# Performance work log

Measured on AMD Instinct MI355X. Metric: run time of the kernel, lower is better.

## Reference

```python
import jax, jax.numpy as jnp
import numpy as np

NEIGHBOUR = 3  # matches init_kwargs['neighbour']


def _conv2d(x, w, b=None, stride=1, pad=0):
    out = jax.lax.conv_general_dilated(
        x, w, (stride, stride), [(pad, pad), (pad, pad)],
        dimension_numbers=('NCHW', 'OIHW', 'NCHW'))
    if b is not None:
        out = out + b[None, :, None, None]
    return out


def _warp(x, offset, wg_w, wg_b, conv_w):
    """Deformable bilinear warp: offsets -> 4 corner gathers -> modulate -> regroup -> strided conv."""
    k = NEIGHBOUR
    N = k * k
    B, C, H, W = x.shape
    m = jax.nn.sigmoid(_conv2d(x, wg_w, wg_b, 1, 1))          # [B,N,H,W] modulation gate
    xp = jnp.pad(x, ((0, 0), (0, 0), (1, 1), (1, 1)))         # zero pad -> [B,C,H+2,W+2]
    Hp, Wp = H + 2, W + 2
    r = jnp.arange(-(k - 1) // 2, (k - 1) // 2 + 1, dtype=x.dtype)
    pnx, pny = jnp.meshgrid(r, r, indexing='ij')              # kernel-neighbour offsets p_n
    # absolute sampling positions in padded coords (p_0 starts at 1 due to padding)
    p0x = jnp.arange(1, H + 1, dtype=x.dtype)[None, :, None, None]
    p0y = jnp.arange(1, W + 1, dtype=x.dtype)[None, None, :, None]
    off = offset.transpose(0, 2, 3, 1)                        # [B,H,W,2N]; first N = x, last N = y
    px = p0x + pnx.ravel()[None, None, None, :] + off[..., :N]  # [B,H,W,N]
    py = p0y + pny.ravel()[None, None, None, :] + off[..., N:]
    fx = jnp.floor(jax.lax.stop_gradient(px))                 # p.detach().floor()
    fy = jnp.floor(jax.lax.stop_gradient(py))
    qx_lt = jnp.clip(fx, 0, Hp - 1)
    qy_lt = jnp.clip(fy, 0, Wp - 1)
    qx_rb = jnp.clip(fx + 1, 0, Hp - 1)
    qy_rb = jnp.clip(fy + 1, 0, Wp - 1)
    px = jnp.clip(px, 0, Hp - 1)
    py = jnp.clip(py, 0, Wp - 1)
    # bilinear weights (same algebra as the torch code)
    g_lt = (1 + (qx_lt - px)) * (1 + (qy_lt - py))
    g_rb = (1 - (qx_rb - px)) * (1 - (qy_rb - py))
    g_lb = (1 + (qx_lt - px)) * (1 - (qy_rb - py))
    g_rt = (1 - (qx_rb - px)) * (1 + (qy_lt - py))
    ix_lt = qx_lt.astype(jnp.int32); iy_lt = qy_lt.astype(jnp.int32)
    ix_rb = qx_rb.astype(jnp.int32); iy_rb = qy_rb.astype(jnp.int32)
    x_flat = xp.reshape(B, C, Hp * Wp)

    def gather(ix, iy):
        idx = (ix * Wp + iy).reshape(B, 1, H * W * N)
        return jnp.take_along_axis(x_flat, idx, axis=-1).reshape(B, C, H, W, N)

    xw = (g_lt[:, None] * gather(ix_lt, iy_lt)
          + g_rb[:, None] * gather(ix_rb, iy_rb)
          + g_lb[:, None] * gather(ix_lt, iy_rb)
          + g_rt[:, None] * gather(ix_rb, iy_lt))              # [B,C,H,W,N]
    xw = xw * m.transpose(0, 2, 3, 1)[:, None]                 # modulation, broadcast over C
    # regroup [B,C,H,W,k,k] -> [B,C,H*k,W*k] (matches _reshape_x_warped ordering)
    xw = xw.reshape(B, C, H, W, k, k).transpose(0, 1, 2, 4, 3, 5).reshape(B, C, H * k, W * k)
    return _conv2d(xw, conv_w, None, stride=k, pad=0)          # grouped-back strided conv


def setup_inputs() -> dict:
    B, C, MH, H, W = 4, 64, 18, 128, 128  # MH = 2*neighbour^2
    key = jax.random.key(0)
    ks = jax.random.split(key, 12)
    f32 = jnp.float32
    s = 0.05  # weight scale to keep gates unsaturated
    return {
        'x_t': jax.random.normal(ks[0], (B, C, H, W), f32),
        'pre_offset': jax.random.normal(ks[1], (B, MH, H, W), f32),
        'mean': jax.random.normal(ks[2], (B, MH, H, W), f32),
        'upd_w': s * jax.random.normal(ks[3], (MH, C + MH, 3, 3), f32),
        'upd_b': s * jax.random.normal(ks[4], (MH,), f32),
        'rst_w': s * jax.random.normal(ks[5], (MH, C + MH, 3, 3), f32),
        'rst_b': s * jax.random.normal(ks[6], (MH,), f32),
        'out_w': s * jax.random.normal(ks[7], (MH, C + MH, 3, 3), f32),
        'out_b': s * jax.random.normal(ks[8], (MH,), f32),
        'wg_w': s * jax.random.normal(ks[9], (9, C, 3, 3), f32),
        'wg_b': s * jax.random.normal(ks[10], (9,), f32),
        'warp_conv_w': s * jax.random.normal(ks[11], (C, C, 3, 3), f32),
    }


def reference(x_t, pre_offset, mean, upd_w, upd_b, rst_w, rst_b, out_w, out_b,
              wg_w, wg_b, warp_conv_w):
    stacked = jnp.concatenate([x_t, pre_offset], axis=1)
    update_gate = jax.nn.sigmoid(_conv2d(stacked, upd_w, upd_b, 1, 1))
    reset_gate = jax.nn.sigmoid(_conv2d(stacked, rst_w, rst_b, 1, 1))
    cand = jnp.tanh(_conv2d(jnp.concatenate([x_t, pre_offset * reset_gate], axis=1), out_w, out_b, 1, 1))
    offset = pre_offset * (1 - update_gate) + cand * update_gate
    mean_new = mean + 0.5 * (pre_offset - mean)
    offset = offset + mean_new
    x_out = _warp(x_t, offset, wg_w, wg_b, warp_conv_w)
    return (x_out, offset, mean_new)
```

## Files before the change

### kernel.cpp

```cpp
#include <hip/hip_runtime.h>
#include <hip/hip_bf16.h>
#include <math.h>

#define Bn  4
#define Cc  64
#define MHc 18
#define Hh  128
#define Wd  128
#define HW  (Hh*Wd)
#define Np  9
#define HP  130
#define WP  130
#define XPE (HP*WP*Cc)
#define PPE (HP*WP*32)
#define KX  576
#define KP  288
#define KT  (KX+KP)

typedef __attribute__((ext_vector_type(8))) short short8;
typedef __attribute__((ext_vector_type(4))) float float4v;

__device__ __forceinline__ float bf2f(__hip_bfloat16 x) { return __bfloat162float(x); }
__device__ __forceinline__ __hip_bfloat16 f2bf(float x) { return __float2bfloat16(x); }
__device__ __forceinline__ float sigm(float x) { return 1.f / (1.f + expf(-x)); }
__device__ __forceinline__ float s2f(short s) {
  return __uint_as_float(((unsigned)(unsigned short)s) << 16);
}
__device__ __forceinline__ short f2bs(float x) {
  __hip_bfloat16 h = __float2bfloat16(x);
  return *reinterpret_cast<short*>(&h);
}

#define NW1 (64*KT)
#define NW2 (32*KP)
#define NW3 (Cc*Cc*Np)

__global__ __launch_bounds__(256)
void k_prep(const float* __restrict__ x, const float* __restrict__ po,
            const float* __restrict__ upd_w, const float* __restrict__ rst_w,
            const float* __restrict__ out_w, const float* __restrict__ wg_w,
            const float* __restrict__ wcw,
            __hip_bfloat16* __restrict__ xp, __hip_bfloat16* __restrict__ pp,
            __hip_bfloat16* __restrict__ wall, __hip_bfloat16* __restrict__ w2,
            __hip_bfloat16* __restrict__ wt) {
  __shared__ float tile[16][65];
  int blk = blockIdx.x;
  int t = threadIdx.x;
  if (blk < 4096) {
    int wtile = blk & 7;
    int h = (blk >> 3) & 127;
    int b = blk >> 10;
    int w0 = wtile * 16;
    int wa = t & 15, cq = t >> 4;
    #pragma unroll
    for (int j = 0; j < 4; ++j) {
      int c = cq * 4 + j;
      tile[wa][c] = x[(b*Cc + c)*HW + h*Wd + w0 + wa];
    }
    __syncthreads();
    int cb = t & 63, wq = t >> 6;
    #pragma unroll
    for (int j = 0; j < 4; ++j) {
      int w = wq * 4 + j;
      xp[b*XPE + ((h+1)*WP + (w0 + w + 1))*Cc + cb] = f2bf(tile[w][cb]);
    }
  } else if (blk < 4608) {
    int pb = blk - 4096;
    int h = pb & 127;
    int b = pb >> 7;
    int w = t & 127;
    int half = t >> 7;
    for (int j = 0; j < 9; ++j) {
      int ch = half * 9 + j;
      float v = po[(b*MHc + ch)*HW + h*Wd + w];
      pp[b*PPE + ((h+1)*WP + (w+1))*32 + ch] = f2bf(v);
    }
  } else {
    int idx = (blk - 4608) * 256 + t;
    if (idx < NW1) {
      int k  = idx % KT;
      int gr = idx / KT;
      float v = 0.f;
      if (k < KX) {
        int n = k >> 6, ci = k & 63;
        if      (gr < 18) v = upd_w[(gr*(Cc+MHc) + ci)*9 + n];
        else if (gr < 36) v = rst_w[((gr-18)*(Cc+MHc) + ci)*9 + n];
        else if (gr < 54) v = out_w[((gr-36)*(Cc+MHc) + ci)*9 + n];
        else if (gr < 63) v = wg_w[((gr-54)*Cc + ci)*9 + n];
      } else {
        int kk = k - KX;
        int n = kk >> 5, jc = kk & 31;
        if (jc < 18) {
          if      (gr < 18) v = upd_w[(gr*(Cc+MHc) + Cc + jc)*9 + n];
          else if (gr < 36) v = rst_w[((gr-18)*(Cc+MHc) + Cc + jc)*9 + n];
        }
      }
      wall[idx] = f2bf(v);
    } else if (idx < NW1 + NW2) {
      int i2 = idx - NW1;
      int k  = i2 % KP;
      int oc = i2 / KP;
      int n = k >> 5, jc = k & 31;
      float v = (oc < 18 && jc < 18) ? out_w[(oc*(Cc+MHc) + Cc + jc)*9 + n] : 0.f;
      w2[i2] = f2bf(v);
    } else if (idx < NW1 + NW2 + NW3) {
      int i3 = idx - NW1 - NW2;
      int k  = i3 % 576;
      int co = i3 / 576;
      wt[i3] = f2bf(wcw[(co*Cc + (k & 63))*9 + (k >> 6)]);
    }
  }
}

__global__ __launch_bounds__(256)
void k_gates(const __hip_bfloat16* __restrict__ xpad,
             const __hip_bfloat16* __restrict__ popad,
             const __hip_bfloat16* __restrict__ wall,
             const float* __restrict__ po,
             const float* __restrict__ upd_b,
             const float* __restrict__ rst_b,
             const float* __restrict__ out_b,
             const float* __restrict__ wg_b,
             float* __restrict__ u_out,
             float* __restrict__ cx_out,
             __hip_bfloat16* __restrict__ ropad,
             __hip_bfloat16* __restrict__ m_t) {
  __shared__ __align__(16) char winx[6912];
  __shared__ __align__(16) char winp[3456];
  __shared__ __align__(16) __hip_bfloat16 roL[16][32];
  int blk = blockIdx.x;
  int wtile = blk & 7;
  int h = (blk >> 3) & 127;
  int b = blk >> 10;
  int w0 = wtile * 16;
  int lane = threadIdx.x & 63;
  int wave = threadIdx.x >> 6;
  int t = threadIdx.x;

  ((unsigned int*)roL)[t] = 0u;

  const __hip_bfloat16* xpb = xpad + b * XPE;
  const __hip_bfloat16* ppb = popad + b * PPE;

  for (int i = t; i < 432; i += 256) {
    int r = i / 144, cidx = i - r * 144;
    short8 v = *reinterpret_cast<const short8*>(
        xpb + ((h + r) * WP + w0) * Cc + cidx * 8);
    int o = i * 16;
    *reinterpret_cast<short8*>(winx + (o ^ (((o >> 7) & 7) << 4))) = v;
  }
  if (t < 216) {
    int r = t / 72, cidx = t - r * 72;
    short8 v = *reinterpret_cast<const short8*>(
        ppb + ((h + r) * WP + w0) * 32 + cidx * 8);
    int o = t * 16;
    *reinterpret_cast<short8*>(winp + (o ^ (((o >> 6) & 3) << 4))) = v;
  }
  __syncthreads();

  int mrow = lane & 15;
  int quad = lane >> 4;
  int cotile = wave * 16;
  float4v acc = {0.f, 0.f, 0.f, 0.f};
  #pragma unroll
  for (int ks = 0; ks < KT/32; ++ks) {
    short8 a = *reinterpret_cast<const short8*>(
        wall + (cotile + mrow) * KT + ks * 32 + quad * 8);
    short8 bfr;
    if (ks < 18) {
      int n = ks >> 1;
      int rowidx = (n / 3) * 18 + mrow + (n % 3);
      int lin = rowidx * 128 + (ks & 1) * 64 + quad * 16;
      bfr = *reinterpret_cast<const short8*>(winx + (lin ^ ((rowidx & 7) << 4)));
    } else {
      int n = ks - 18;
      int rowidx = (n / 3) * 18 + mrow + (n % 3);
      int lin = rowidx * 64 + quad * 16;
      bfr = *reinterpret_cast<const short8*>(winp + (lin ^ ((rowidx & 3) << 4)));
    }
    acc = __builtin_amdgcn_mfma_f32_16x16x32_bf16(a, bfr, acc, 0, 0, 0);
  }

  int sp = h * Wd + w0 + mrow;
  #pragma unroll
  for (int r = 0; r < 4; ++r) {
    int gr = cotile + quad * 4 + r;
    float v = acc[r];
    if (gr < 18) {
      u_out[(b*MHc + gr)*HW + sp] = sigm(v + upd_b[gr]);
    } else if (gr < 36) {
      int oc = gr - 18;
      float rr = sigm(v + rst_b[oc]);
      roL[mrow][oc] = f2bf(rr * po[(b*MHc + oc)*HW + sp]);
    } else if (gr < 54) {
      int oc = gr - 36;
      cx_out[(b*MHc + oc)*HW + sp] = v + out_b[oc];
    } else if (gr < 63) {
      int nn = gr - 54;
      m_t[(b*HW + sp)*9 + nn] = f2bf(sigm(v + wg_b[nn]));
    }
  }
  __syncthreads();
  unsigned int* dst = (unsigned int*)(ropad + b*PPE + ((h+1)*WP + (w0+1))*32);
  dst[t] = ((unsigned int*)roL)[t];
}

__global__ __launch_bounds__(256)
void k_fuse(const __hip_bfloat16* __restrict__ xpad,
            const __hip_bfloat16* __restrict__ ropad,
            const __hip_bfloat16* __restrict__ w2,
            const __hip_bfloat16* __restrict__ wt,
            const __hip_bfloat16* __restrict__ m_t,
            const float* __restrict__ po,
            const float* __restrict__ mean,
            float* __restrict__ out_off,
            float* __restrict__ out_mn,
            float* __restrict__ out_x) {
  __shared__ __align__(16) char lbuf[16*584*2];
  __shared__ float offL[16][18];
  __shared__ float mL[16][9];
  __shared__ __align__(16) float gw[144][4];
  __shared__ __align__(16) int   gb[144][2];
  auto xw = (__hip_bfloat16(*)[584])lbuf;

  int blk = blockIdx.x;
  int wtile = blk & 7;
  int h = (blk >> 3) & 127;
  int b = blk >> 10;
  int w0 = wtile * 16;
  int lane = threadIdx.x & 63;
  int wave = threadIdx.x >> 6;
  int t = threadIdx.x;

  const __hip_bfloat16* rpb = ropad + b * PPE;
  if (t < 216) {
    int r = t / 72, cidx = t - r * 72;
    short8 v = *reinterpret_cast<const short8*>(
        rpb + ((h + r) * WP + w0) * 32 + cidx * 8);
    int o = t * 16;
    *reinterpret_cast<short8*>(lbuf + (o ^ (((o >> 6) & 3) << 4))) = v;
  }
  __syncthreads();

  int mrow = lane & 15;
  int quad = lane >> 4;

  if (wave < 2) {
    float4v acc = {0.f, 0.f, 0.f, 0.f};
    #pragma unroll
    for (int ks = 0; ks < KP/32; ++ks) {
      short8 a = *reinterpret_cast<const short8*>(
          w2 + (wave*16 + mrow) * KP + ks * 32 + quad * 8);
      int rowidx = (ks / 3) * 18 + mrow + (ks % 3);
      int lin = rowidx * 64 + quad * 16;
      short8 bfr = *reinterpret_cast<const short8*>(
          lbuf + (lin ^ ((rowidx & 3) << 4)));
      acc = __builtin_amdgcn_mfma_f32_16x16x32_bf16(a, bfr, acc, 0, 0, 0);
    }
    int sp = h * Wd + w0 + mrow;
    #pragma unroll
    for (int r = 0; r < 4; ++r) {
      int gr = wave*16 + quad * 4 + r;
      if (gr < 18) {
        int gi = (b*MHc + gr)*HW + sp;
        float cand = tanhf(out_off[gi] + acc[r]);
        float u = out_mn[gi];
        float p = po[gi];
        float mn = 0.5f * (mean[gi] + p);
        float off = p * (1.f - u) + cand * u + mn;
        out_off[gi] = off;
        out_mn[gi]  = mn;
        offL[mrow][gr] = off;
      }
    }
  } else {
    int base = (wave - 2) * 64 + lane;
    #pragma unroll
    for (int rep = 0; rep < 2; ++rep) {
      int id = base + rep * 128;
      if (id < 144) {
        int px = id / 9, n = id % 9;
        mL[px][n] = bf2f(m_t[(b*HW + h*Wd + w0 + px)*9 + n]);
      }
    }
  }
  __syncthreads();

  if (t < 144) {
    int px = t / 9;
    int n = t - px * 9;
    int wp = w0 + px;
    float ox = offL[px][n];
    float oy = offL[px][9 + n];
    float mnv = mL[px][n];
    float px_ = (float)(h + 1) + (float)(n / 3 - 1) + ox;
    float py_ = (float)(wp + 1) + (float)(n % 3 - 1) + oy;
    float fx = floorf(px_), fy = floorf(py_);
    float xlt = fminf(fmaxf(fx,       0.f), 129.f);
    float ylt = fminf(fmaxf(fy,       0.f), 129.f);
    float xrb = fminf(fmaxf(fx + 1.f, 0.f), 129.f);
    float yrb = fminf(fmaxf(fy + 1.f, 0.f), 129.f);
    float pxc = fminf(fmaxf(px_, 0.f), 129.f);
    float pyc = fminf(fmaxf(py_, 0.f), 129.f);
    float glt = (1.f + xlt - pxc) * (1.f + ylt - pyc);
    float grb = (1.f - xrb + pxc) * (1.f - yrb + pyc);
    float glb = (1.f + xlt - pxc) * (1.f - yrb + pyc);
    float grt = (1.f - xrb + pxc) * (1.f + ylt - pyc);
    int ixl = (int)xlt, iyl = (int)ylt, ixr = (int)xrb, iyr = (int)yrb;
    bool yAdj = (iyr == iyl + 1);
    gw[t][0] = (glt + (yAdj ? 0.f : glb)) * mnv;
    gw[t][1] = (yAdj ? glb : 0.f) * mnv;
    gw[t][2] = (grt + (yAdj ? 0.f : grb)) * mnv;
    gw[t][3] = (yAdj ? grb : 0.f) * mnv;
    gb[t][0] = (ixl * WP + iyl) * Cc;
    gb[t][1] = (ixr * WP + iyl) * Cc;
  }
  __syncthreads();

  const __hip_bfloat16* xpb = xpad + b * XPE;
  for (int it = t; it < 1152; it += 256) {
    int q  = it >> 3;
    int c0 = (it & 7) * 8;
    float4v g = *reinterpret_cast<const float4v*>(gw[q]);
    int bL = gb[q][0], bR = gb[q][1];
    short8 l0 = *reinterpret_cast<const short8*>(xpb + bL + c0);
    short8 l1 = *reinterpret_cast<const short8*>(xpb + bL + 64 + c0);
    short8 r0 = *reinterpret_cast<const short8*>(xpb + bR + c0);
    short8 r1 = *reinterpret_cast<const short8*>(xpb + bR + 64 + c0);
    short8 ov;
    #pragma unroll
    for (int j = 0; j < 8; ++j) {
      float vv = g.x * s2f(l0[j]);
      vv = fmaf(g.y, s2f(l1[j]), vv);
      vv = fmaf(g.z, s2f(r0[j]), vv);
      vv = fmaf(g.w, s2f(r1[j]), vv);
      ov[j] = f2bs(vv);
    }
    int pl = q / 9;
    int n  = q - pl * 9;
    *reinterpret_cast<short8*>(&xw[pl][n * 64 + c0]) = ov;
  }
  __syncthreads();

  int cotile = wave * 16;
  float4v acc = {0.f, 0.f, 0.f, 0.f};
  for (int ks = 0; ks < 18; ++ks) {
    short8 a = *reinterpret_cast<const short8*>(
        wt + (cotile + mrow) * 576 + ks * 32 + quad * 8);
    short8 bfr = *reinterpret_cast<const short8*>(
        &xw[mrow][ks * 32 + quad * 8]);
    acc = __builtin_amdgcn_mfma_f32_16x16x32_bf16(a, bfr, acc, 0, 0, 0);
  }
  #pragma unroll
  for (int r = 0; r < 4; ++r) {
    int co = cotile + quad * 4 + r;
    out_x[((b * Cc + co) * Hh + h) * Wd + w0 + mrow] = acc[r];
  }
}

__global__ void f_convAB(const float* __restrict__ x, const float* __restrict__ po,
                         const float* __restrict__ wA, const float* __restrict__ bA,
                         const float* __restrict__ wB, const float* __restrict__ bB,
                         float* __restrict__ u_scr, float* __restrict__ ro_scr) {
  int idx = blockIdx.x * 256 + threadIdx.x;
  if (idx >= Bn * MHc * HW) return;
  int w = idx & 127, h = (idx >> 7) & 127, oc = (idx >> 14) % MHc, b = idx / (MHc*HW);
  float accA = bA[oc], accB = bB[oc];
  const float* xb = x + b*Cc*HW; const float* pb = po + b*MHc*HW;
  for (int ic = 0; ic < Cc + MHc; ++ic) {
    const float* src = (ic < Cc) ? (xb + ic*HW) : (pb + (ic-Cc)*HW);
    const float* wa = wA + (oc*(Cc+MHc)+ic)*9; const float* wb = wB + (oc*(Cc+MHc)+ic)*9;
    for (int kh = 0; kh < 3; ++kh) { int hh = h+kh-1; if ((unsigned)hh >= Hh) continue;
      for (int kw = 0; kw < 3; ++kw) { int ww = w+kw-1; if ((unsigned)ww >= Wd) continue;
        float v = src[hh*Wd+ww]; accA += v*wa[kh*3+kw]; accB += v*wb[kh*3+kw]; } }
  }
  u_scr[idx] = sigm(accA); ro_scr[idx] = sigm(accB) * pb[oc*HW + h*Wd + w];
}
__global__ void f_convC(const float* __restrict__ x, const float* __restrict__ po,
                        const float* __restrict__ mean, const float* __restrict__ wC,
                        const float* __restrict__ bC, const float* __restrict__ u_scr,
                        const float* __restrict__ ro_scr, float* __restrict__ out_off,
                        float* __restrict__ out_mean) {
  int idx = blockIdx.x * 256 + threadIdx.x;
  if (idx >= Bn * MHc * HW) return;
  int w = idx & 127, h = (idx >> 7) & 127, oc = (idx >> 14) % MHc, b = idx / (MHc*HW);
  float acc = bC[oc];
  const float* xb = x + b*Cc*HW; const float* rb = ro_scr + b*MHc*HW;
  for (int ic = 0; ic < Cc + MHc; ++ic) {
    const float* src = (ic < Cc) ? (xb + ic*HW) : (rb + (ic-Cc)*HW);
    const float* wv = wC + (oc*(Cc+MHc)+ic)*9;
    for (int kh = 0; kh < 3; ++kh) { int hh = h+kh-1; if ((unsigned)hh >= Hh) continue;
      for (int kw = 0; kw < 3; ++kw) { int ww = w+kw-1; if ((unsigned)ww >= Wd) continue;
        acc += src[hh*Wd+ww]*wv[kh*3+kw]; } }
  }
  float cand = tanhf(acc); float u = u_scr[idx]; float p = po[idx];
  float mn = 0.5f*(mean[idx]+p);
  out_off[idx] = p*(1.f-u)+cand*u+mn; out_mean[idx] = mn;
}
__global__ __launch_bounds__(256)
void f_warp(const float* __restrict__ x, const float* __restrict__ off_f,
            const float* __restrict__ wg, const float* __restrict__ bg,
            const float* __restrict__ wc, float* __restrict__ out) {
  __shared__ float mred[4][Np][64]; __shared__ float mval[4][Np];
  __shared__ float xwv[4][Np][64];
  int lane = threadIdx.x & 63, wave = threadIdx.x >> 6;
  int p = blockIdx.x * 4 + wave;
  int b = p >> 14, rem = p & 16383, h = rem >> 7, w = rem & 127;
  const float* xc = x + (b*Cc + lane)*HW;
  float part[Np];
  for (int n = 0; n < Np; ++n) part[n] = 0.f;
  for (int kh = 0; kh < 3; ++kh) { int hh = h+kh-1; if ((unsigned)hh >= Hh) continue;
    for (int kw = 0; kw < 3; ++kw) { int ww = w+kw-1; if ((unsigned)ww >= Wd) continue;
      float v = xc[hh*Wd+ww];
      for (int n = 0; n < Np; ++n) part[n] += v*wg[(n*Cc+lane)*9+kh*3+kw]; } }
  for (int n = 0; n < Np; ++n) mred[wave][n][lane] = part[n];
  __syncthreads();
  if (lane < Np) { float s = bg[lane];
    for (int c = 0; c < Cc; ++c) s += mred[wave][lane][c];
    mval[wave][lane] = sigm(s); }
  __syncthreads();
  const float* offb = off_f + b*MHc*HW; int sp = h*Wd + w;
  for (int n = 0; n < Np; ++n) {
    float px = (float)(h+1) + (float)(n/3-1) + offb[n*HW+sp];
    float py = (float)(w+1) + (float)(n%3-1) + offb[(9+n)*HW+sp];
    float fxq = floorf(px), fyq = floorf(py);
    float xlt = fminf(fmaxf(fxq,0.f),129.f), ylt = fminf(fmaxf(fyq,0.f),129.f);
    float xrb = fminf(fmaxf(fxq+1.f,0.f),129.f), yrb = fminf(fmaxf(fyq+1.f,0.f),129.f);
    float pxc = fminf(fmaxf(px,0.f),129.f), pyc = fminf(fmaxf(py,0.f),129.f);
    float glt = (1.f+xlt-pxc)*(1.f+ylt-pyc), grb = (1.f-xrb+pxc)*(1.f-yrb+pyc);
    float glb = (1.f+xlt-pxc)*(1.f-yrb+pyc), grt = (1.f-xrb+pxc)*(1.f+ylt-pyc);
    int ixl=(int)xlt, iyl=(int)ylt, ixr=(int)xrb, iyr=(int)yrb;
    float vlt=0.f,vrb=0.f,vlb=0.f,vrt=0.f;
    if (ixl>=1&&ixl<=Hh&&iyl>=1&&iyl<=Wd) vlt = xc[(ixl-1)*Wd+(iyl-1)];
    if (ixr>=1&&ixr<=Hh&&iyr>=1&&iyr<=Wd) vrb = xc[(ixr-1)*Wd+(iyr-1)];
    if (ixl>=1&&ixl<=Hh&&iyr>=1&&iyr<=Wd) vlb = xc[(ixl-1)*Wd+(iyr-1)];
    if (ixr>=1&&ixr<=Hh&&iyl>=1&&iyl<=Wd) vrt = xc[(ixr-1)*Wd+(iyl-1)];
    xwv[wave][n][lane] = (glt*vlt+grb*vrb+glb*vlb+grt*vrt)*mval[wave][n];
  }
  __syncthreads();
  float acc = 0.f;
  for (int c = 0; c < Cc; ++c)
    for (int n = 0; n < Np; ++n)
      acc += xwv[wave][n][c]*wc[(lane*Cc+c)*9+n];
  out[(b*Cc+lane)*HW + h*Wd + w] = acc;
}

extern "C" void kernel_launch(void* const* d_in, const int* in_sizes, int n_in,
                              void* d_out, int out_size, void* d_ws, size_t ws_size,
                              hipStream_t stream) {
  (void)in_sizes; (void)n_in; (void)out_size;
  const float* x_t   = (const float*)d_in[0];
  const float* po    = (const float*)d_in[1];
  const float* mean  = (const float*)d_in[2];
  const float* upd_w = (const float*)d_in[3];
  const float* upd_b = (const float*)d_in[4];
  const float* rst_w = (const float*)d_in[5];
  const float* rst_b = (const float*)d_in[6];
  const float* out_w = (const float*)d_in[7];
  const float* out_b = (const float*)d_in[8];
  const float* wg_w  = (const float*)d_in[9];
  const float* wg_b  = (const float*)d_in[10];
  const float* wcw   = (const float*)d_in[11];

  float* out_x   = (float*)d_out;
  float* out_off = out_x + 4194304;
  float* out_mn  = out_off + 1179648;

  char* ws = (char*)d_ws;
  __hip_bfloat16* xpad  = (__hip_bfloat16*)(ws + 0);
  __hip_bfloat16* popad = (__hip_bfloat16*)(ws + 8652800);
  __hip_bfloat16* ropad = (__hip_bfloat16*)(ws + 12979200);
  __hip_bfloat16* wall  = (__hip_bfloat16*)(ws + 17305600);
  __hip_bfloat16* w2    = (__hip_bfloat16*)(ws + 17416192);
  __hip_bfloat16* wt_bf = (__hip_bfloat16*)(ws + 17434624);
  __hip_bfloat16* m_t   = (__hip_bfloat16*)(ws + 17508352);
  const size_t WS_NEED = 18688000;

  if (ws_size >= WS_NEED) {
    hipMemsetAsync(d_ws, 0, 17305600, stream);
    hipLaunchKernelGGL(k_prep,  dim3(5004), dim3(256), 0, stream,
                       x_t, po, upd_w, rst_w, out_w, wg_w, wcw,
                       xpad, popad, wall, w2, wt_bf);
    hipLaunchKernelGGL(k_gates, dim3(4096), dim3(256), 0, stream,
                       xpad, popad, wall, po, upd_b, rst_b, out_b, wg_b,
                       out_mn, out_off, ropad, m_t);
    hipLaunchKernelGGL(k_fuse,  dim3(4096), dim3(256), 0, stream,
                       xpad, ropad, w2, wt_bf, m_t, po, mean,
                       out_off, out_mn, out_x);
  } else {
    float* u_scr  = out_x;
    float* cx_scr = out_x + 1179648;
    hipLaunchKernelGGL(f_convAB, dim3(4608), dim3(256), 0, stream,
                       x_t, po, upd_w, upd_b, rst_w, rst_b, u_scr, cx_scr);
    hipLaunchKernelGGL(f_convC,  dim3(4608), dim3(256), 0, stream,
                       x_t, po, mean, out_w, out_b, u_scr, cx_scr,
                       out_off, out_mn);
    hipLaunchKernelGGL(f_warp,   dim3(16384), dim3(256), 0, stream,
                       x_t, out_off, wg_w, wg_b, wcw, out_x);
  }
}
```

Measured before the change: 203.1 us.

## Restructure k_fuse so each wave owns 16 pixels without block barriers

k_fuse now runs 128-thread blocks, and each wave handles its own 16-pixel strip end to end. A wave computes the candidate conv with MFMA straight from global ropad, then the bilinear coefficients in per-wave shared slots. It builds the warped B-fragments in registers and feeds them directly into four MFMA accumulators covering all 64 output channels. This removes the staged LDS tiles and all __syncthreads, trading them for redundant global weight loads per wave and higher register pressure.

```diff
diff --git a/kernel.cpp b/kernel.cpp
--- a/kernel.cpp
+++ b/kernel.cpp
@@ -205,7 +205,7 @@
   dst[t] = ((unsigned int*)roL)[t];
 }
 
-__global__ __launch_bounds__(256)
+__global__ __launch_bounds__(128)
 void k_fuse(const __hip_bfloat16* __restrict__ xpad,
             const __hip_bfloat16* __restrict__ ropad,
             const __hip_bfloat16* __restrict__ w2,
@@ -216,145 +216,137 @@
             float* __restrict__ out_off,
             float* __restrict__ out_mn,
             float* __restrict__ out_x) {
-  __shared__ __align__(16) char lbuf[16*584*2];
-  __shared__ float offL[16][18];
-  __shared__ float mL[16][9];
-  __shared__ __align__(16) float gw[144][4];
-  __shared__ __align__(16) int   gb[144][2];
-  auto xw = (__hip_bfloat16(*)[584])lbuf;
+  __shared__ float offW[2][16][18];
+  __shared__ __align__(16) float gwW[2][144][4];
+  __shared__ __align__(8)  int   gbW[2][144][2];
 
   int blk = blockIdx.x;
-  int wtile = blk & 7;
-  int h = (blk >> 3) & 127;
-  int b = blk >> 10;
-  int w0 = wtile * 16;
+  int wtile = blk & 3;
+  int h = (blk >> 2) & 127;
+  int b = blk >> 9;
   int lane = threadIdx.x & 63;
-  int wave = threadIdx.x >> 6;
-  int t = threadIdx.x;
-
-  const __hip_bfloat16* rpb = ropad + b * PPE;
-  if (t < 216) {
-    int r = t / 72, cidx = t - r * 72;
-    short8 v = *reinterpret_cast<const short8*>(
-        rpb + ((h + r) * WP + w0) * 32 + cidx * 8);
-    int o = t * 16;
-    *reinterpret_cast<short8*>(lbuf + (o ^ (((o >> 6) & 3) << 4))) = v;
-  }
-  __syncthreads();
+  int wv = threadIdx.x >> 6;
+  int wq0 = wtile * 32 + wv * 16;
 
   int mrow = lane & 15;
   int quad = lane >> 4;
 
-  if (wave < 2) {
-    float4v acc = {0.f, 0.f, 0.f, 0.f};
-    #pragma unroll
-    for (int ks = 0; ks < KP/32; ++ks) {
-      short8 a = *reinterpret_cast<const short8*>(
-          w2 + (wave*16 + mrow) * KP + ks * 32 + quad * 8);
-      int rowidx = (ks / 3) * 18 + mrow + (ks % 3);
-      int lin = rowidx * 64 + quad * 16;
-      short8 bfr = *reinterpret_cast<const short8*>(
-          lbuf + (lin ^ ((rowidx & 3) << 4)));
-      acc = __builtin_amdgcn_mfma_f32_16x16x32_bf16(a, bfr, acc, 0, 0, 0);
-    }
-    int sp = h * Wd + w0 + mrow;
+  const __hip_bfloat16* rpb = ropad + b * PPE;
+  float4v acc2a = {0.f,0.f,0.f,0.f}, acc2b = {0.f,0.f,0.f,0.f};
+  #pragma unroll
+  for (int ks = 0; ks < 9; ++ks) {
+    short8 bfr = *reinterpret_cast<const short8*>(
+        rpb + ((h + ks/3) * WP + wq0 + mrow + ks%3) * 32 + quad * 8);
+    short8 a0 = *reinterpret_cast<const short8*>(
+        w2 + mrow * KP + ks * 32 + quad * 8);
+    short8 a1 = *reinterpret_cast<const short8*>(
+        w2 + (16 + mrow) * KP + ks * 32 + quad * 8);
+    acc2a = __builtin_amdgcn_mfma_f32_16x16x32_bf16(a0, bfr, acc2a, 0, 0, 0);
+    acc2b = __builtin_amdgcn_mfma_f32_16x16x32_bf16(a1, bfr, acc2b, 0, 0, 0);
+  }
+
+  int sp = h * Wd + wq0 + mrow;
+  #pragma unroll
+  for (int am = 0; am < 2; ++am) {
+    float4v av = am ? acc2b : acc2a;
     #pragma unroll
     for (int r = 0; r < 4; ++r) {
-      int gr = wave*16 + quad * 4 + r;
+      int gr = am*16 + quad * 4 + r;
       if (gr < 18) {
         int gi = (b*MHc + gr)*HW + sp;
-        float cand = tanhf(out_off[gi] + acc[r]);
+        float cand = tanhf(out_off[gi] + av[r]);
         float u = out_mn[gi];
         float p = po[gi];
         float mn = 0.5f * (mean[gi] + p);
         float off = p * (1.f - u) + cand * u + mn;
         out_off[gi] = off;
         out_mn[gi]  = mn;
-        offL[mrow][gr] = off;
+        offW[wv][mrow][gr] = off;
       }
     }
-  } else {
-    int base = (wave - 2) * 64 + lane;
-    #pragma unroll
-    for (int rep = 0; rep < 2; ++rep) {
-      int id = base + rep * 128;
-      if (id < 144) {
-        int px = id / 9, n = id % 9;
-        mL[px][n] = bf2f(m_t[(b*HW + h*Wd + w0 + px)*9 + n]);
-      }
-    }
-  }
-  __syncthreads();
-
-  if (t < 144) {
-    int px = t / 9;
-    int n = t - px * 9;
-    int wp = w0 + px;
-    float ox = offL[px][n];
-    float oy = offL[px][9 + n];
-    float mnv = mL[px][n];
-    float px_ = (float)(h + 1) + (float)(n / 3 - 1) + ox;
-    float py_ = (float)(wp + 1) + (float)(n % 3 - 1) + oy;
-    float fx = floorf(px_), fy = floorf(py_);
-    float xlt = fminf(fmaxf(fx,       0.f), 129.f);
-    float ylt = fminf(fmaxf(fy,       0.f), 129.f);
-    float xrb = fminf(fmaxf(fx + 1.f, 0.f), 129.f);
-    float yrb = fminf(fmaxf(fy + 1.f, 0.f), 129.f);
-    float pxc = fminf(fmaxf(px_, 0.f), 129.f);
-    float pyc = fminf(fmaxf(py_, 0.f), 129.f);
-    float glt = (1.f + xlt - pxc) * (1.f + ylt - pyc);
-    float grb = (1.f - xrb + pxc) * (1.f - yrb + pyc);
-    float glb = (1.f + xlt - pxc) * (1.f - yrb + pyc);
-    float grt = (1.f - xrb + pxc) * (1.f + ylt - pyc);
-    int ixl = (int)xlt, iyl = (int)ylt, ixr = (int)xrb, iyr = (int)yrb;
-    bool yAdj = (iyr == iyl + 1);
-    gw[t][0] = (glt + (yAdj ? 0.f : glb)) * mnv;
-    gw[t][1] = (yAdj ? glb : 0.f) * mnv;
-    gw[t][2] = (grt + (yAdj ? 0.f : grb)) * mnv;
-    gw[t][3] = (yAdj ? grb : 0.f) * mnv;
-    gb[t][0] = (ixl * WP + iyl) * Cc;
-    gb[t][1] = (ixr * WP + iyl) * Cc;
-  }
-  __syncthreads();
+  }
+
+  const __hip_bfloat16* mtb = m_t + (size_t)(b*HW + h*Wd + wq0) * 9;
+  #pragma unroll
+  for (int rep = 0; rep < 3; ++rep) {
+    int id = lane + rep * 64;
+    if (id < 144) {
+      int px = id / 9;
+      int n = id - px * 9;
+      int wp = wq0 + px;
+      float ox = offW[wv][px][n];
+      float oy = offW[wv][px][9 + n];
+      float mnv = bf2f(mtb[px * 9 + n]);
+      float px_ = (float)(h + 1) + (float)(n / 3 - 1) + ox;
+      float py_ = (float)(wp + 1) + (float)(n % 3 - 1) + oy;
+      float fx = floorf(px_), fy = floorf(py_);
+      float xlt = fminf(fmaxf(fx,       0.f), 129.f);
+      float ylt = fminf(fmaxf(fy,       0.f), 129.f);
+      float xrb = fminf(fmaxf(fx + 1.f, 0.f), 129.f);
+      float yrb = fminf(fmaxf(fy + 1.f, 0.f), 129.f);
+      float pxc = fminf(fmaxf(px_, 0.f), 129.f);
+      float pyc = fminf(fmaxf(py_, 0.f), 129.f);
+      float glt = (1.f + xlt - pxc) * (1.f + ylt - pyc);
+      float grb = (1.f - xrb + pxc) * (1.f - yrb + pyc);
+      float glb = (1.f + xlt - pxc) * (1.f - yrb + pyc);
+      float grt = (1.f - xrb + pxc) * (1.f + ylt - pyc);
+      int ixl = (int)xlt, iyl = (int)ylt, ixr = (int)xrb, iyr = (int)yrb;
+      bool yAdj = (iyr == iyl + 1);
+      gwW[wv][id][0] = (glt + (yAdj ? 0.f : glb)) * mnv;
+      gwW[wv][id][1] = (yAdj ? glb : 0.f) * mnv;
+      gwW[wv][id][2] = (grt + (yAdj ? 0.f : grb)) * mnv;
+      gwW[wv][id][3] = (yAdj ? grb : 0.f) * mnv;
+      gbW[wv][id][0] = (ixl * WP + iyl) * Cc;
+      gbW[wv][id][1] = (ixr * WP + iyl) * Cc;
+    }
+  }
 
   const __hip_bfloat16* xpb = xpad + b * XPE;
-  for (int it = t; it < 1152; it += 256) {
-    int q  = it >> 3;
-    int c0 = (it & 7) * 8;
-    float4v g = *reinterpret_cast<const float4v*>(gw[q]);
-    int bL = gb[q][0], bR = gb[q][1];
-    short8 l0 = *reinterpret_cast<const short8*>(xpb + bL + c0);
-    short8 l1 = *reinterpret_cast<const short8*>(xpb + bL + 64 + c0);
-    short8 r0 = *reinterpret_cast<const short8*>(xpb + bR + c0);
-    short8 r1 = *reinterpret_cast<const short8*>(xpb + bR + 64 + c0);
-    short8 ov;
+  float4v acc0 = {0.f,0.f,0.f,0.f}, acc1 = {0.f,0.f,0.f,0.f};
+  float4v acc2 = {0.f,0.f,0.f,0.f}, acc3 = {0.f,0.f,0.f,0.f};
+  int q0 = mrow * 9;
+  int cbase = quad * 8;
+  #pragma unroll
+  for (int ks = 0; ks < 18; ++ks) {
+    int q = q0 + (ks >> 1);
+    float4v g = *reinterpret_cast<const float4v*>(gwW[wv][q]);
+    int co = ((ks & 1) << 5) + cbase;
+    int bL = gbW[wv][q][0] + co;
+    int bR = gbW[wv][q][1] + co;
+    short8 l0 = *reinterpret_cast<const short8*>(xpb + bL);
+    short8 l1 = *reinterpret_cast<const short8*>(xpb + bL + 64);
+    short8 r0 = *reinterpret_cast<const short8*>(xpb + bR);
+    short8 r1 = *reinterpret_cast<const short8*>(xpb + bR + 64);
+    short8 bfr;
     #pragma unroll
     for (int j = 0; j < 8; ++j) {
       float vv = g.x * s2f(l0[j]);
       vv = fmaf(g.y, s2f(l1[j]), vv);
       vv = fmaf(g.z, s2f(r0[j]), vv);
       vv = fmaf(g.w, s2f(r1[j]), vv);
-      ov[j] = f2bs(vv);
-    }
-    int pl = q / 9;
-    int n  = q - pl * 9;
-    *reinterpret_cast<short8*>(&xw[pl][n * 64 + c0]) = ov;
-  }
-  __syncthreads();
-
-  int cotile = wave * 16;
-  float4v acc = {0.f, 0.f, 0.f, 0.f};
-  for (int ks = 0; ks < 18; ++ks) {
-    short8 a = *reinterpret_cast<const short8*>(
-        wt + (cotile + mrow) * 576 + ks * 32 + quad * 8);
-    short8 bfr = *reinterpret_cast<const short8*>(
-        &xw[mrow][ks * 32 + quad * 8]);
-    acc = __builtin_amdgcn_mfma_f32_16x16x32_bf16(a, bfr, acc, 0, 0, 0);
+      bfr[j] = f2bs(vv);
+    }
+    short8 a0 = *reinterpret_cast<const short8*>(
+        wt + (0*16 + mrow) * 576 + ks * 32 + cbase);
+    short8 a1 = *reinterpret_cast<const short8*>(
+        wt + (1*16 + mrow) * 576 + ks * 32 + cbase);
+    short8 a2 = *reinterpret_cast<const short8*>(
+        wt + (2*16 + mrow) * 576 + ks * 32 + cbase);
+    short8 a3 = *reinterpret_cast<const short8*>(
+        wt + (3*16 + mrow) * 576 + ks * 32 + cbase);
+    acc0 = __builtin_amdgcn_mfma_f32_16x16x32_bf16(a0, bfr, acc0, 0, 0, 0);
+    acc1 = __builtin_amdgcn_mfma_f32_16x16x32_bf16(a1, bfr, acc1, 0, 0, 0);
+    acc2 = __builtin_amdgcn_mfma_f32_16x16x32_bf16(a2, bfr, acc2, 0, 0, 0);
+    acc3 = __builtin_amdgcn_mfma_f32_16x16x32_bf16(a3, bfr, acc3, 0, 0, 0);
   }
   #pragma unroll
   for (int r = 0; r < 4; ++r) {
-    int co = cotile + quad * 4 + r;
-    out_x[((b * Cc + co) * Hh + h) * Wd + w0 + mrow] = acc[r];
+    float4v* accp[4] = {&acc0, &acc1, &acc2, &acc3};
+    #pragma unroll
+    for (int ct = 0; ct < 4; ++ct) {
+      int co = ct * 16 + quad * 4 + r;
+      out_x[((b * Cc + co) * Hh + h) * Wd + wq0 + mrow] = (*accp[ct])[r];
+    }
   }
 }
 
@@ -484,7 +476,7 @@
     hipLaunchKernelGGL(k_gates, dim3(4096), dim3(256), 0, stream,
                        xpad, popad, wall, po, upd_b, rst_b, out_b, wg_b,
                        out_mn, out_off, ropad, m_t);
-    hipLaunchKernelGGL(k_fuse,  dim3(4096), dim3(256), 0, stream,
+    hipLaunchKernelGGL(k_fuse,  dim3(2048), dim3(128), 0, stream,
                        xpad, ropad, w2, wt_bf, m_t, po, mean,
                        out_off, out_mn, out_x);
   } else {
```

Result: slower. 215.2 us (+6.0%).

## Batch global loads ahead of use and transpose modulation layout across kernels

Applied to the files above, without the earlier changes.

Vectorizes the input transpose in the prep kernel (float4 reads, packed bf16 pair writes) and hoists global loads into registers before computation in the conv, fuse, and gather stages. The gather loop issues all corner loads for five iterations up front, then blends, which puts more loads in flight. The modulation buffer moves to a channel-major layout, so its load in the fuse kernel is coalesced and runs before the first barrier. The cost is higher register pressure, which may lower occupancy.

```diff
diff --git a/kernel.cpp b/kernel.cpp
--- a/kernel.cpp
+++ b/kernel.cpp
@@ -29,6 +29,9 @@
 __device__ __forceinline__ short f2bs(float x) {
   __hip_bfloat16 h = __float2bfloat16(x);
   return *reinterpret_cast<short*>(&h);
+}
+__device__ __forceinline__ unsigned pack2(float lo, float hi) {
+  return (unsigned)(unsigned short)f2bs(lo) | ((unsigned)(unsigned short)f2bs(hi) << 16);
 }
 
 #define NW1 (64*KT)
@@ -51,18 +54,21 @@
     int h = (blk >> 3) & 127;
     int b = blk >> 10;
     int w0 = wtile * 16;
-    int wa = t & 15, cq = t >> 4;
+    int c = t >> 2, wq = t & 3;
+    float4v v = *reinterpret_cast<const float4v*>(
+        &x[(b*Cc + c)*HW + h*Wd + w0 + wq*4]);
+    tile[wq*4+0][c] = v.x;
+    tile[wq*4+1][c] = v.y;
+    tile[wq*4+2][c] = v.z;
+    tile[wq*4+3][c] = v.w;
+    __syncthreads();
+    int cb2 = t & 31, wrow = t >> 5;
     #pragma unroll
-    for (int j = 0; j < 4; ++j) {
-      int c = cq * 4 + j;
-      tile[wa][c] = x[(b*Cc + c)*HW + h*Wd + w0 + wa];
-    }
-    __syncthreads();
-    int cb = t & 63, wq = t >> 6;
-    #pragma unroll
-    for (int j = 0; j < 4; ++j) {
-      int w = wq * 4 + j;
-      xp[b*XPE + ((h+1)*WP + (w0 + w + 1))*Cc + cb] = f2bf(tile[w][cb]);
+    for (int j = 0; j < 2; ++j) {
+      int w = wrow + 8*j;
+      unsigned val = pack2(tile[w][cb2*2], tile[w][cb2*2+1]);
+      *reinterpret_cast<unsigned*>(
+          &xp[b*XPE + ((h+1)*WP + (w0 + w + 1))*Cc + cb2*2]) = val;
     }
   } else if (blk < 4608) {
     int pb = blk - 4096;
@@ -70,11 +76,13 @@
     int b = pb >> 7;
     int w = t & 127;
     int half = t >> 7;
-    for (int j = 0; j < 9; ++j) {
-      int ch = half * 9 + j;
-      float v = po[(b*MHc + ch)*HW + h*Wd + w];
-      pp[b*PPE + ((h+1)*WP + (w+1))*32 + ch] = f2bf(v);
-    }
+    float v[9];
+    #pragma unroll
+    for (int j = 0; j < 9; ++j)
+      v[j] = po[(b*MHc + half*9 + j)*HW + h*Wd + w];
+    #pragma unroll
+    for (int j = 0; j < 9; ++j)
+      pp[b*PPE + ((h+1)*WP + (w+1))*32 + half*9 + j] = f2bf(v[j]);
   } else {
     int idx = (blk - 4608) * 256 + t;
     if (idx < NW1) {
@@ -142,19 +150,30 @@
   const __hip_bfloat16* xpb = xpad + b * XPE;
   const __hip_bfloat16* ppb = popad + b * PPE;
 
-  for (int i = t; i < 432; i += 256) {
-    int r = i / 144, cidx = i - r * 144;
-    short8 v = *reinterpret_cast<const short8*>(
-        xpb + ((h + r) * WP + w0) * Cc + cidx * 8);
-    int o = i * 16;
-    *reinterpret_cast<short8*>(winx + (o ^ (((o >> 7) & 7) << 4))) = v;
-  }
-  if (t < 216) {
-    int r = t / 72, cidx = t - r * 72;
-    short8 v = *reinterpret_cast<const short8*>(
-        ppb + ((h + r) * WP + w0) * 32 + cidx * 8);
+  int r0 = t / 144, c0i = t - r0 * 144;
+  short8 vx0 = *reinterpret_cast<const short8*>(
+      xpb + ((h + r0) * WP + w0) * Cc + c0i * 8);
+  bool h2 = (t < 176);
+  short8 vx1;
+  int i1 = t + 256, r1 = i1 / 144, c1i = i1 - r1 * 144;
+  if (h2) vx1 = *reinterpret_cast<const short8*>(
+      xpb + ((h + r1) * WP + w0) * Cc + c1i * 8);
+  bool hp = (t < 216);
+  short8 vp;
+  int rp = t / 72, cpi = t - rp * 72;
+  if (hp) vp = *reinterpret_cast<const short8*>(
+      ppb + ((h + rp) * WP + w0) * 32 + cpi * 8);
+  {
     int o = t * 16;
-    *reinterpret_cast<short8*>(winp + (o ^ (((o >> 6) & 3) << 4))) = v;
+    *reinterpret_cast<short8*>(winx + (o ^ (((o >> 7) & 7) << 4))) = vx0;
+  }
+  if (h2) {
+    int o = i1 * 16;
+    *reinterpret_cast<short8*>(winx + (o ^ (((o >> 7) & 7) << 4))) = vx1;
+  }
+  if (hp) {
+    int o = t * 16;
+    *reinterpret_cast<short8*>(winp + (o ^ (((o >> 6) & 3) << 4))) = vp;
   }
   __syncthreads();
 
@@ -182,6 +201,13 @@
   }
 
   int sp = h * Wd + w0 + mrow;
+  float pv[4];
+  #pragma unroll
+  for (int r = 0; r < 4; ++r) {
+    int gr = cotile + quad * 4 + r;
+    if (gr >= 18 && gr < 36)
+      pv[r] = po[(b*MHc + (gr-18))*HW + sp];
+  }
   #pragma unroll
   for (int r = 0; r < 4; ++r) {
     int gr = cotile + quad * 4 + r;
@@ -191,13 +217,13 @@
     } else if (gr < 36) {
       int oc = gr - 18;
       float rr = sigm(v + rst_b[oc]);
-      roL[mrow][oc] = f2bf(rr * po[(b*MHc + oc)*HW + sp]);
+      roL[mrow][oc] = f2bf(rr * pv[r]);
     } else if (gr < 54) {
       int oc = gr - 36;
       cx_out[(b*MHc + oc)*HW + sp] = v + out_b[oc];
     } else if (gr < 63) {
       int nn = gr - 54;
-      m_t[(b*HW + sp)*9 + nn] = f2bf(sigm(v + wg_b[nn]));
+      m_t[nn*(Bn*HW) + b*HW + sp] = f2bf(sigm(v + wg_b[nn]));
     }
   }
   __syncthreads();
@@ -220,8 +246,9 @@
   __shared__ float offL[16][18];
   __shared__ float mL[16][9];
   __shared__ __align__(16) float gw[144][4];
-  __shared__ __align__(16) int   gb[144][2];
-  auto xw = (__hip_bfloat16(*)[584])lbuf;
+  __shared__ __align__(16) int   ga[144][2];
+  auto shro = (__hip_bfloat16(*)[KP+8])lbuf;
+  auto xw   = (__hip_bfloat16(*)[584])lbuf;
 
   int blk = blockIdx.x;
   int wtile = blk & 7;
@@ -239,6 +266,10 @@
         rpb + ((h + r) * WP + w0) * 32 + cidx * 8);
     int o = t * 16;
     *reinterpret_cast<short8*>(lbuf + (o ^ (((o >> 6) & 3) << 4))) = v;
+  }
+  if (t < 144) {
+    int n = t >> 4, px = t & 15;
+    mL[px][n] = bf2f(m_t[n*(Bn*HW) + b*HW + h*Wd + w0 + px]);
   }
   __syncthreads();
 
@@ -258,29 +289,29 @@
       acc = __builtin_amdgcn_mfma_f32_16x16x32_bf16(a, bfr, acc, 0, 0, 0);
     }
     int sp = h * Wd + w0 + mrow;
+    float ov[4], uv[4], pv[4], mv[4];
+    int gil[4];
+    #pragma unroll
+    for (int r = 0; r < 4; ++r) {
+      int gr = wave*16 + quad * 4 + r;
+      gil[r] = (b*MHc + gr)*HW + sp;
+      if (gr < 18) {
+        ov[r] = out_off[gil[r]];
+        uv[r] = out_mn[gil[r]];
+        pv[r] = po[gil[r]];
+        mv[r] = mean[gil[r]];
+      }
+    }
     #pragma unroll
     for (int r = 0; r < 4; ++r) {
       int gr = wave*16 + quad * 4 + r;
       if (gr < 18) {
-        int gi = (b*MHc + gr)*HW + sp;
-        float cand = tanhf(out_off[gi] + acc[r]);
-        float u = out_mn[gi];
-        float p = po[gi];
-        float mn = 0.5f * (mean[gi] + p);
-        float off = p * (1.f - u) + cand * u + mn;
-        out_off[gi] = off;
-        out_mn[gi]  = mn;
+        float cand = tanhf(ov[r] + acc[r]);
+        float mn = 0.5f * (mv[r] + pv[r]);
+        float off = pv[r] * (1.f - uv[r]) + cand * uv[r] + mn;
+        out_off[gil[r]] = off;
+        out_mn[gil[r]]  = mn;
         offL[mrow][gr] = off;
-      }
-    }
-  } else {
-    int base = (wave - 2) * 64 + lane;
-    #pragma unroll
-    for (int rep = 0; rep < 2; ++rep) {
-      int id = base + rep * 128;
-      if (id < 144) {
-        int px = id / 9, n = id % 9;
-        mL[px][n] = bf2f(m_t[(b*HW + h*Wd + w0 + px)*9 + n]);
       }
     }
   }
@@ -312,38 +343,57 @@
     gw[t][1] = (yAdj ? glb : 0.f) * mnv;
     gw[t][2] = (grt + (yAdj ? 0.f : grb)) * mnv;
     gw[t][3] = (yAdj ? grb : 0.f) * mnv;
-    gb[t][0] = (ixl * WP + iyl) * Cc;
-    gb[t][1] = (ixr * WP + iyl) * Cc;
+    ga[t][0] = (ixl * WP + iyl) * Cc;
+    ga[t][1] = (ixr * WP + iyl) * Cc;
   }
   __syncthreads();
 
   const __hip_bfloat16* xpb = xpad + b * XPE;
-  for (int it = t; it < 1152; it += 256) {
-    int q  = it >> 3;
-    int c0 = (it & 7) * 8;
-    float4v g = *reinterpret_cast<const float4v*>(gw[q]);
-    int bL = gb[q][0], bR = gb[q][1];
-    short8 l0 = *reinterpret_cast<const short8*>(xpb + bL + c0);
-    short8 l1 = *reinterpret_cast<const short8*>(xpb + bL + 64 + c0);
-    short8 r0 = *reinterpret_cast<const short8*>(xpb + bR + c0);
-    short8 r1 = *reinterpret_cast<const short8*>(xpb + bR + 64 + c0);
-    short8 ov;
-    #pragma unroll
-    for (int j = 0; j < 8; ++j) {
-      float vv = g.x * s2f(l0[j]);
-      vv = fmaf(g.y, s2f(l1[j]), vv);
-      vv = fmaf(g.z, s2f(r0[j]), vv);
-      vv = fmaf(g.w, s2f(r1[j]), vv);
-      ov[j] = f2bs(vv);
-    }
-    int pl = q / 9;
-    int n  = q - pl * 9;
-    *reinterpret_cast<short8*>(&xw[pl][n * 64 + c0]) = ov;
+  short8 A0[5], A1[5], A2[5], A3[5];
+  float4v Gq[5];
+  int qq[5];
+  #pragma unroll
+  for (int rep = 0; rep < 5; ++rep) {
+    int it = t + rep * 256;
+    bool ok = (rep < 4) || (t < 128);
+    if (ok) {
+      int q = it >> 3, c0 = (it & 7) * 8;
+      qq[rep] = q;
+      Gq[rep] = *reinterpret_cast<const float4v*>(gw[q]);
+      int bL = ga[q][0] + c0, bR = ga[q][1] + c0;
+      A0[rep] = *reinterpret_cast<const short8*>(xpb + bL);
+      A1[rep] = *reinterpret_cast<const short8*>(xpb + bL + 64);
+      A2[rep] = *reinterpret_cast<const short8*>(xpb + bR);
+      A3[rep] = *reinterpret_cast<const short8*>(xpb + bR + 64);
+    }
+  }
+  #pragma unroll
+  for (int rep = 0; rep < 5; ++rep) {
+    int it = t + rep * 256;
+    bool ok = (rep < 4) || (t < 128);
+    if (ok) {
+      float4v g = Gq[rep];
+      short8 ov;
+      #pragma unroll
+      for (int j = 0; j < 8; ++j) {
+        float vv = g.x * s2f(A0[rep][j]);
+        vv = fmaf(g.y, s2f(A1[rep][j]), vv);
+        vv = fmaf(g.z, s2f(A2[rep][j]), vv);
+        vv = fmaf(g.w, s2f(A3[rep][j]), vv);
+        ov[j] = f2bs(vv);
+      }
+      int q = qq[rep];
+      int pl = q / 9;
+      int n  = q - pl * 9;
+      int c0 = (it & 7) * 8;
+      *reinterpret_cast<short8*>(&xw[pl][n * 64 + c0]) = ov;
+    }
   }
   __syncthreads();
 
   int cotile = wave * 16;
   float4v acc = {0.f, 0.f, 0.f, 0.f};
+  #pragma unroll
   for (int ks = 0; ks < 18; ++ks) {
     short8 a = *reinterpret_cast<const short8*>(
         wt + (cotile + mrow) * 576 + ks * 32 + quad * 8);
```

Result: slower. 209.7 us (+3.2%).
